# Optimization experiments

Measured on AMD Instinct MI355X. Metric: run time of the kernel, lower is better.

Reference implementation:

```python
import jax, jax.numpy as jnp
import numpy as np

K = 256      # embedding size k
STATE = 128  # latent state size
IN = 64      # external input size
OBS = 64     # observation size
L = 512      # sequence length (time-major)
B = 256      # batch size


def _glorot(key, shape):
    return jax.random.normal(key, shape, dtype=jnp.float32) / float(np.sqrt(shape[0]))


def setup_inputs():
    key = jax.random.key(0)
    ks = jax.random.split(key, 12)
    p = {}
    p["external_input_seq"] = jax.random.normal(ks[0], (L, B, IN), dtype=jnp.float32)
    p["observations_seq"] = jax.random.normal(ks[1], (L, B, OBS), dtype=jnp.float32)
    p["eps"] = jax.random.normal(ks[2], (L, B, STATE), dtype=jnp.float32)  # reparam noise
    # PreProcess: Linear + tanh
    p["Wu"] = _glorot(ks[3], (IN, K)); p["bu"] = jnp.zeros((K,), jnp.float32)
    p["Wx"] = _glorot(ks[4], (OBS, K)); p["bx"] = jnp.zeros((K,), jnp.float32)
    # input_rnn: vanilla tanh RNN, 1 layer, k -> k
    p["W_ih"] = _glorot(ks[5], (K, K)); p["b_ih"] = jnp.zeros((K,), jnp.float32)
    p["W_hh"] = _glorot(ks[6], (K, K)); p["b_hh"] = jnp.zeros((K,), jnp.float32)
    # posterior_a_layer: MLP(2k, k, k, 1) = Linear -> tanh -> Linear
    p["Wa1"] = _glorot(ks[7], (2 * K, K)); p["ba1"] = jnp.zeros((K,), jnp.float32)
    p["Wa2"] = _glorot(ks[8], (K, K)); p["ba2"] = jnp.zeros((K,), jnp.float32)

    def dblock_params(k1, in_dim, hid, out):
        kk = jax.random.split(k1, 4)
        return (_glorot(kk[0], (in_dim, hid)), jnp.zeros((hid,), jnp.float32),
                _glorot(kk[1], (in_dim, hid)), jnp.zeros((hid,), jnp.float32),
                _glorot(kk[2], (hid, out)), jnp.zeros((out,), jnp.float32),
                _glorot(kk[3], (hid, out)), jnp.zeros((out,), jnp.float32))

    names = ["f1_W", "f1_b", "f2_W", "f2_b", "mu_W", "mu_b", "ls_W", "ls_b"]
    for pref, kk in (("post_", ks[9]), ("prior_", ks[10])):
        vals = dblock_params(kk, STATE + K, 2 * K, STATE)
        for n, v in zip(names, vals):
            p[pref + n] = v
    return p


def _dblock(x, f1_W, f1_b, f2_W, f2_b, mu_W, mu_b, ls_W, ls_b):
    # TD-VAE DBlock: gated hidden, then mu / logsigma heads
    t = jnp.tanh(x @ f1_W + f1_b) * jax.nn.sigmoid(x @ f2_W + f2_b)
    return t @ mu_W + mu_b, t @ ls_W + ls_b


def reference(external_input_seq, observations_seq, eps, Wu, bu, Wx, bx,
              W_ih, b_ih, W_hh, b_hh, Wa1, ba1, Wa2, ba2,
              post_f1_W, post_f1_b, post_f2_W, post_f2_b, post_mu_W, post_mu_b, post_ls_W, post_ls_b,
              prior_f1_W, prior_f1_b, prior_f2_W, prior_f2_b, prior_mu_W, prior_mu_b, prior_ls_W, prior_ls_b):
    batch = external_input_seq.shape[1]
    u_emb = jnp.tanh(external_input_seq @ Wu + bu)   # [L,B,K]
    x_emb = jnp.tanh(observations_seq @ Wx + bx)     # [L,B,K]

    # input_rnn (tanh RNN) over time, d0 = 0 (memory_state=None)
    def rnn_step(d, x):
        d_new = jnp.tanh(x @ W_ih + b_ih + d @ W_hh + b_hh)
        return d_new, d_new
    d0 = jnp.zeros((batch, W_hh.shape[0]), dtype=u_emb.dtype)
    dn, d_seq = jax.lax.scan(rnn_step, d0, u_emb)    # dn [B,K], d_seq [L,B,K]

    # posterior_a_layer: pointwise MLP; flip(0) then flip(0) is a no-op for a pointwise map
    ad = jnp.concatenate([d_seq, x_emb], axis=-1)    # [L,B,2K]
    a_seq = jnp.tanh(ad @ Wa1 + ba1) @ Wa2 + ba2     # [L,B,K]

    state_size = post_mu_W.shape[1]
    z0 = jnp.zeros((batch, state_size), dtype=u_emb.dtype)

    def step(z_prev, inp):
        a_t, d_t, e_t = inp
        mean_res, logsigma = _dblock(jnp.concatenate([z_prev, a_t], axis=-1),
                                     post_f1_W, post_f1_b, post_f2_W, post_f2_b,
                                     post_mu_W, post_mu_b, post_ls_W, post_ls_b)
        prior_mean = _dblock(jnp.concatenate([z_prev, d_t], axis=-1),
                             prior_f1_W, prior_f1_b, prior_f2_W, prior_f2_b,
                             prior_mu_W, prior_mu_b, prior_ls_W, prior_ls_b)[0]
        mu = prior_mean + mean_res
        # cov = diag(exp(logsigma)) -> std = exp(0.5*logsigma); reparameterized sample
        z_new = mu + jnp.exp(0.5 * logsigma) * e_t
        return z_new, (mu, logsigma)

    zn, (state_mu, state_logsigma) = jax.lax.scan(step, z0, (a_seq, d_seq, eps))
    return state_mu, state_logsigma, dn, zn
```

## Files before the change

kernel.cpp:

```cpp
#include <hip/hip_runtime.h>

#define LSEQ 512
#define BATCH 256
#define KDIM 256
#define STATE 128

using f32x4  = __attribute__((ext_vector_type(4))) float;
using short8 = __attribute__((ext_vector_type(8))) short;
using u32x2  = __attribute__((ext_vector_type(2))) unsigned int;
using u32x4  = __attribute__((ext_vector_type(4))) unsigned int;

__device__ __forceinline__ float bf2f(unsigned short u){
  return __uint_as_float(((unsigned int)u) << 16);
}
__device__ __forceinline__ unsigned short f2bf(float f){
  unsigned int u = __float_as_uint(f);
  u += 0x7FFFu + ((u >> 16) & 1u);
  return (unsigned short)(u >> 16);
}
__device__ __forceinline__ float fast_tanh(float x){
  float ax = fabsf(x);
  float e  = __expf(2.0f * ax);
  float t  = 1.0f - 2.0f / (e + 1.0f);
  return copysignf(t, x);
}
__device__ __forceinline__ float fast_sig(float x){
  return 1.0f / (1.0f + __expf(-x));
}
__device__ __forceinline__ f32x4 mfma16(short8 a, short8 b, f32x4 c){
  return __builtin_amdgcn_mfma_f32_16x16x32_bf16(a, b, c, 0, 0, 0);
}

__device__ __forceinline__ int swz128 (int b){ return b ^ ((((b >> 7) & 7) << 4)); }
__device__ __forceinline__ int swz256 (int b){ return b ^ ((((b >> 8) & 7) << 4)); }
__device__ __forceinline__ int swz512 (int b){ return b ^ ((((b >> 9) & 7) << 4)); }

__device__ __forceinline__ void st_b128_ic(void* p, u32x4 v){
  asm volatile("global_store_dwordx4 %0, %1, off sc0 sc1" :: "v"(p), "v"(v) : "memory");
}
__device__ __forceinline__ void st_b64_ic(void* p, u32x2 v){
  asm volatile("global_store_dwordx2 %0, %1, off sc0 sc1" :: "v"(p), "v"(v) : "memory");
}
#define LD2_IC(dst, p) asm volatile("global_load_dwordx2 %0, %1, off sc0 sc1" : "=v"(dst) : "v"(p) : "memory")

__device__ __forceinline__ f32x4 cvt4(u32x2 q){
  f32x4 r;
  r[0] = __uint_as_float(q[0] << 16);
  r[1] = __uint_as_float(q[0] & 0xFFFF0000u);
  r[2] = __uint_as_float(q[1] << 16);
  r[3] = __uint_as_float(q[1] & 0xFFFF0000u);
  return r;
}

struct WDesc { const float* src; unsigned short* dst; int K, N, ld, rowoff, coloff; };
struct WDescs { WDesc d[24]; };

__global__ __launch_bounds__(256,4) void convert_weights(WDescs ds){
  WDesc w = ds.d[blockIdx.y];
  int total = w.K * w.N;
  int idx = blockIdx.x * 256 + threadIdx.x;
  if (idx < total){
    int n = idx / w.K;
    int k = idx - n * w.K;
    w.dst[idx] = f2bf(w.src[(size_t)(w.rowoff + k) * w.ld + w.coloff + n]);
  }
}

__global__ __launch_bounds__(256,1) void init_flags(int* flags){
  flags[blockIdx.x * 256 + threadIdx.x] = 0;
}

struct GArg {
  const void* A; const unsigned short* Bt; const float* bias; const float* bias2;
  unsigned short* C; int lda, ldc, coff, K, act, a_f32;
};
struct GArgs { GArg g[4]; };

__global__ __launch_bounds__(256,2) void gemm_multi(GArgs args){
  GArg ga = args.g[blockIdx.z];
  __shared__ __align__(16) unsigned short lsA[128*64];
  __shared__ __align__(16) unsigned short lsB[128*64];
  const int tid  = threadIdx.x;
  const int wave = tid >> 6, lane = tid & 63;
  const int col_l = lane & 15, rgrp = lane >> 4;
  const int m0 = blockIdx.x * 128, n0 = blockIdx.y * 128;
  const int wm = (wave >> 1) * 64, wn = (wave & 1) * 64;

  f32x4 acc[4][4];
  const f32x4 z4 = {0.f,0.f,0.f,0.f};
  #pragma unroll
  for (int i=0;i<4;i++){ acc[i][0]=z4; acc[i][1]=z4; acc[i][2]=z4; acc[i][3]=z4; }

  const int srow = tid >> 1;
  const int sbe  = (tid & 1) * 32;

  for (int k0 = 0; k0 < ga.K; k0 += 64){
    uint4 av[4], bv[4];
    if (ga.a_f32){
      const float* Ap = (const float*)ga.A + (size_t)(m0 + srow) * ga.lda + k0 + sbe;
      uint4 fv[8];
      #pragma unroll
      for (int i=0;i<8;i++) fv[i] = *(const uint4*)((const char*)Ap + i*16);
      #pragma unroll
      for (int i=0;i<4;i++){
        const float* f = (const float*)&fv[i*2];
        uint4 o;
        o.x = (unsigned)f2bf(f[0]) | ((unsigned)f2bf(f[1]) << 16);
        o.y = (unsigned)f2bf(f[2]) | ((unsigned)f2bf(f[3]) << 16);
        o.z = (unsigned)f2bf(f[4]) | ((unsigned)f2bf(f[5]) << 16);
        o.w = (unsigned)f2bf(f[6]) | ((unsigned)f2bf(f[7]) << 16);
        av[i] = o;
      }
    } else {
      const unsigned short* Ap = (const unsigned short*)ga.A + (size_t)(m0 + srow) * ga.lda + k0 + sbe;
      #pragma unroll
      for (int i=0;i<4;i++) av[i] = *(const uint4*)((const char*)Ap + i*16);
    }
    const unsigned short* Bp = ga.Bt + (size_t)(n0 + srow) * ga.K + k0 + sbe;
    #pragma unroll
    for (int i=0;i<4;i++) bv[i] = *(const uint4*)((const char*)Bp + i*16);

    __syncthreads();
    #pragma unroll
    for (int i=0;i<4;i++){
      *(uint4*)((char*)lsA + swz128(srow*128 + sbe*2 + i*16)) = av[i];
      *(uint4*)((char*)lsB + swz128(srow*128 + sbe*2 + i*16)) = bv[i];
    }
    __syncthreads();
    #pragma unroll
    for (int kk=0; kk<2; kk++){
      short8 af[4], bfr[4];
      #pragma unroll
      for (int mt=0; mt<4; mt++)
        af[mt] = *(const short8*)((const char*)lsA + swz128((wm + mt*16 + col_l)*128 + kk*64 + rgrp*16));
      #pragma unroll
      for (int nt=0; nt<4; nt++)
        bfr[nt] = *(const short8*)((const char*)lsB + swz128((wn + nt*16 + col_l)*128 + kk*64 + rgrp*16));
      #pragma unroll
      for (int mt=0; mt<4; mt++)
        #pragma unroll
        for (int nt=0; nt<4; nt++)
          acc[mt][nt] = mfma16(af[mt], bfr[nt], acc[mt][nt]);
    }
  }
  #pragma unroll
  for (int nt=0; nt<4; nt++){
    int col = n0 + wn + nt*16 + col_l;
    const float* bsrc = (col < 512) ? ga.bias : ga.bias2;
    float bb = bsrc ? bsrc[col & 511] : 0.0f;
    #pragma unroll
    for (int mt=0; mt<4; mt++){
      #pragma unroll
      for (int r=0; r<4; r++){
        int row = m0 + wm + mt*16 + rgrp*4 + r;
        float v = acc[mt][nt][r] + bb;
        if (ga.act == 1) v = fast_tanh(v);
        ga.C[(size_t)row * ga.ldc + ga.coff + col] = f2bf(v);
      }
    }
  }
}

__global__ __launch_bounds__(256,1) void rnn_chunk(
    const unsigned short* __restrict__ rnn_in,
    const unsigned short* __restrict__ Whh_t,
    const float* __restrict__ b_hh,
    unsigned short* __restrict__ cat_d,
    float* __restrict__ dn_out,
    unsigned short* __restrict__ d_state,
    int t0, int nsteps)
{
  __shared__ __align__(16) unsigned short dls[16*256];
  const int tid = threadIdx.x, wave = tid >> 6, lane = tid & 63;
  const int col_l = lane & 15, rgrp = lane >> 4;
  const int brow0 = blockIdx.x * 16;
  const int ncol = wave * 64;

  short8 bfr[4][8];
  #pragma unroll
  for (int nt=0; nt<4; nt++){
    const unsigned short* bp = Whh_t + (size_t)(ncol + nt*16 + col_l) * 256;
    #pragma unroll
    for (int kk=0; kk<8; kk++)
      bfr[nt][kk] = *(const short8*)(bp + kk*32 + rgrp*8);
  }
  float bias[4];
  #pragma unroll
  for (int nt=0; nt<4; nt++) bias[nt] = b_hh[ncol + nt*16 + col_l];

  if (t0 == 0){
    for (int i = tid; i < 16*256; i += 256){
      int row = i >> 8, col = i & 255;
      *(unsigned short*)((char*)dls + swz512(row*512 + col*2)) = 0;
    }
  } else {
    const unsigned short* ds = d_state + (size_t)brow0 * 256;
    for (int i = tid; i < 16*256; i += 256){
      int row = i >> 8, col = i & 255;
      *(unsigned short*)((char*)dls + swz512(row*512 + col*2)) = ds[row*256 + col];
    }
  }
  __syncthreads();

  for (int tl=0; tl<nsteps; tl++){
    unsigned short rv[4][4];
    const unsigned short* rp = rnn_in + (size_t)(tl*BATCH + brow0) * 256;
    #pragma unroll
    for (int nt=0; nt<4; nt++)
      #pragma unroll
      for (int r=0; r<4; r++)
        rv[nt][r] = rp[(size_t)(rgrp*4 + r)*256 + ncol + nt*16 + col_l];

    f32x4 acc[4];
    const f32x4 z4 = {0.f,0.f,0.f,0.f};
    acc[0]=z4; acc[1]=z4; acc[2]=z4; acc[3]=z4;
    #pragma unroll
    for (int kk=0; kk<8; kk++){
      short8 af = *(const short8*)((const char*)dls + swz512((lane & 15)*512 + kk*64 + rgrp*16));
      #pragma unroll
      for (int nt=0; nt<4; nt++)
        acc[nt] = mfma16(af, bfr[nt][kk], acc[nt]);
    }
    __syncthreads();
    #pragma unroll
    for (int nt=0; nt<4; nt++){
      #pragma unroll
      for (int r=0; r<4; r++){
        float h = acc[nt][r] + bf2f(rv[nt][r]) + bias[nt];
        float d = fast_tanh(h);
        int row = rgrp*4 + r, col = ncol + nt*16 + col_l;
        unsigned short db = f2bf(d);
        *(unsigned short*)((char*)dls + swz512(row*512 + col*2)) = db;
        cat_d[(size_t)(tl*BATCH + brow0 + row)*512 + col] = db;
        if (t0 + tl == LSEQ-1) dn_out[(size_t)(brow0 + row)*256 + col] = d;
      }
    }
    __syncthreads();
  }
  unsigned short* dso = d_state + (size_t)brow0 * 256;
  for (int i = tid; i < 16*256; i += 256){
    int row = i >> 8, col = i & 255;
    dso[row*256 + col] = *(const unsigned short*)((const char*)dls + swz512(row*512 + col*2));
  }
}

__global__ __launch_bounds__(512,1) void zrec_mb(
    const unsigned short* __restrict__ preP, const unsigned short* __restrict__ preQ,
    const unsigned short* __restrict__ Wzz,
    const unsigned short* __restrict__ W2,
    const float* __restrict__ pmub, const float* __restrict__ plsb, const float* __restrict__ qmub,
    const float* __restrict__ eps,
    float* __restrict__ out_mu, float* __restrict__ out_ls, float* __restrict__ out_zn,
    unsigned short* __restrict__ z_state,
    unsigned short* __restrict__ mb, int* __restrict__ flags,
    int t0, int nsteps, int fbase)
{
  __shared__ __align__(16) unsigned short zls[16*128];
  __shared__ __align__(16) unsigned short tls[16*256];
  const int tid = threadIdx.x, wave = tid >> 6, lane = tid & 63;
  const int col_l = lane & 15, rgrp = lane >> 4;
  const int bid = blockIdx.x;
  const int c   = (bid >> 3) & 3;
  const int g   = (bid & 7) + ((bid >> 5) << 3);
  const int brow0 = g * 16;
  const int NT2 = (c < 2) ? 2 : 1;

  const unsigned short* pre = (c < 2) ? preP : preQ;
  const int cb = (c & 1) * 256;

  short8 w1[2][2][4];
  {
    const unsigned short* wz = Wzz + (size_t)c * 65536;
    #pragma unroll
    for (int m=0; m<2; m++)
      #pragma unroll
      for (int nt=0; nt<2; nt++){
        int n = wave*32 + nt*16 + col_l;
        #pragma unroll
        for (int kk=0; kk<4; kk++)
          w1[m][nt][kk] = *(const short8*)(wz + (size_t)(m*256 + n)*128 + kk*32 + rgrp*8);
      }
  }
  short8 w2r[2][8];
  {
    const unsigned short* wp = W2 + (size_t)c * 65536;
    #pragma unroll
    for (int nt=0; nt<2; nt++){
      if (nt < NT2){
        int ccol = wave*(16*((c<2)?2:1)) + nt*16;
        int mat = (c < 2) ? (ccol >> 7) : 0;
        int n   = (ccol & 127) + col_l;
        #pragma unroll
        for (int kk=0; kk<8; kk++)
          w2r[nt][kk] = *(const short8*)(wp + (size_t)(mat*128 + n)*256 + kk*32 + rgrp*8);
      }
    }
  }
  int* const myflag = flags + (g*4 + c)*32;

  if (t0 == 0){
    for (int i = tid; i < 16*128; i += 512){
      int row = i >> 7, col = i & 127;
      *(unsigned short*)((char*)zls + swz256(row*256 + col*2)) = 0;
    }
  } else {
    const unsigned short* zs = z_state + (size_t)brow0 * 128;
    for (int i = tid; i < 16*128; i += 512){
      int row = i >> 7, col = i & 127;
      *(unsigned short*)((char*)zls + swz256(row*256 + col*2)) = zs[row*128 + col];
    }
  }
  __syncthreads();

  auto LD_PRE = [&](int tl, unsigned short (&pa_)[2][4], unsigned short (&pb_)[2][4]){
    const unsigned short* bA = pre + ((size_t)tl*BATCH + brow0)*1024 + cb;
    #pragma unroll
    for (int nt=0; nt<2; nt++)
      #pragma unroll
      for (int r=0; r<4; r++){
        int row = rgrp*4 + r, col = wave*32 + nt*16 + col_l;
        pa_[nt][r] = bA[(size_t)row*1024 + col];
        pb_[nt][r] = bA[(size_t)row*1024 + 512 + col];
      }
  };

  const int rrow = tid >> 5;
  const int rc0  = (tid & 31) * 4;
  const f32x4 bp4 = *(const f32x4*)(pmub + rc0);
  const f32x4 bl4 = *(const f32x4*)(plsb + rc0);
  const f32x4 bq4 = *(const f32x4*)(qmub + rc0);

  unsigned short pa0[2][4], pb0[2][4], pa1[2][4], pb1[2][4];
  LD_PRE(0, pa0, pb0);

  const f32x4 z4 = {0.f,0.f,0.f,0.f};
  for (int tl=0; tl<nsteps; ++tl){
    size_t growr = (size_t)(t0+tl)*BATCH + brow0 + rrow;
    f32x4 er = *(const f32x4*)(eps + growr*STATE + rc0);
    int nx = (tl+1 < nsteps) ? tl+1 : tl;
    LD_PRE(nx, pa1, pb1);

    short8 af1[4];
    #pragma unroll
    for (int kk=0; kk<4; kk++)
      af1[kk] = *(const short8*)((const char*)zls + swz256((lane & 15)*256 + kk*64 + rgrp*16));
    f32x4 a1[2][2];
    a1[0][0]=z4; a1[0][1]=z4; a1[1][0]=z4; a1[1][1]=z4;
    #pragma unroll
    for (int kk=0; kk<4; kk++)
      #pragma unroll
      for (int m=0; m<2; m++)
        #pragma unroll
        for (int nt=0; nt<2; nt++)
          a1[m][nt] = mfma16(af1[kk], w1[m][nt][kk], a1[m][nt]);

    #pragma unroll
    for (int nt=0; nt<2; nt++)
      #pragma unroll
      for (int r=0; r<4; r++){
        float h1 = a1[0][nt][r] + bf2f(pa0[nt][r]);
        float h2 = a1[1][nt][r] + bf2f(pb0[nt][r]);
        float tv = fast_tanh(h1) * fast_sig(h2);
        int row = rgrp*4 + r, tcol = wave*32 + nt*16 + col_l;
        *(unsigned short*)((char*)tls + swz512(row*512 + tcol*2)) = f2bf(tv);
      }
    __syncthreads();

    f32x4 a2[2];
    a2[0]=z4; a2[1]=z4;
    #pragma unroll
    for (int kk=0; kk<8; kk++){
      short8 af2 = *(const short8*)((const char*)tls + swz512((lane & 15)*512 + kk*64 + rgrp*16));
      #pragma unroll
      for (int nt=0; nt<2; nt++)
        if (nt < NT2) a2[nt] = mfma16(af2, w2r[nt][kk], a2[nt]);
    }
    __syncthreads();

    if (c < 2){
      #pragma unroll
      for (int nt=0; nt<2; nt++)
        #pragma unroll
        for (int r=0; r<4; r++)
          tls[(rgrp*4 + r)*256 + wave*32 + nt*16 + col_l] = f2bf(a2[nt][r]);
    } else {
      #pragma unroll
      for (int r=0; r<4; r++)
        tls[(rgrp*4 + r)*128 + wave*16 + col_l] = f2bf(a2[0][r]);
    }
    __syncthreads();

    unsigned short* slot = mb + (size_t)((g*2 + (tl & 1))*4 + c)*4096;
    if (c < 2){
      u32x4 v = *(const u32x4*)((const char*)tls + tid*16);
      st_b128_ic(slot + tid*8, v);
    } else {
      u32x2 v = *(const u32x2*)((const char*)tls + tid*8);
      st_b64_ic(slot + tid*4, v);
    }
    asm volatile("s_waitcnt vmcnt(0)" ::: "memory");
    __syncthreads();
    const int target = fbase + tl + 1;
    if (tid == 0)
      __hip_atomic_store(myflag, target, __ATOMIC_RELAXED, __HIP_MEMORY_SCOPE_AGENT);

    if (wave == 7 && lane < 3){
      const int* pf = flags + (g*4 + ((c + 1 + lane) & 3))*32;
      while (__hip_atomic_load(pf, __ATOMIC_RELAXED, __HIP_MEMORY_SCOPE_AGENT) < target)
        __builtin_amdgcn_s_sleep(1);
    }
    __syncthreads();

    const unsigned short* mbb = mb + (size_t)((g*2 + (tl & 1))*4)*4096;
    const unsigned short* s0 = mbb;
    const unsigned short* s1 = mbb + 4096;
    const unsigned short* s2 = mbb + 8192;
    const unsigned short* s3 = mbb + 12288;
    u32x2 q0,q1,q2,q3,q4,q5;
    LD2_IC(q0, s0 + rrow*256 + rc0);
    LD2_IC(q1, s1 + rrow*256 + rc0);
    LD2_IC(q2, s0 + rrow*256 + 128 + rc0);
    LD2_IC(q3, s1 + rrow*256 + 128 + rc0);
    LD2_IC(q4, s2 + rrow*128 + rc0);
    LD2_IC(q5, s3 + rrow*128 + rc0);
    asm volatile("s_waitcnt vmcnt(0)" ::: "memory");
    __builtin_amdgcn_sched_barrier(0);

    f32x4 mup = cvt4(q0) + cvt4(q1);
    f32x4 lsv = cvt4(q2) + cvt4(q3) + bl4;
    f32x4 muq = cvt4(q4) + cvt4(q5);
    f32x4 muv = (muq + bq4) + (mup + bp4);
    f32x4 zv;
    #pragma unroll
    for (int i=0; i<4; i++) zv[i] = muv[i] + __expf(0.5f * lsv[i]) * er[i];

    unsigned int lo = (unsigned)f2bf(zv[0]) | ((unsigned)f2bf(zv[1]) << 16);
    unsigned int hi = (unsigned)f2bf(zv[2]) | ((unsigned)f2bf(zv[3]) << 16);
    uint2 zp; zp.x = lo; zp.y = hi;
    *(uint2*)((char*)zls + swz256(rrow*256 + rc0*2)) = zp;
    if (c == 0){
      *(f32x4*)(out_mu + growr*STATE + rc0) = muv;
      *(f32x4*)(out_ls + growr*STATE + rc0) = lsv;
      if (t0 + tl == LSEQ-1)
        *(f32x4*)(out_zn + ((size_t)(brow0 + rrow))*STATE + rc0) = zv;
    }
    __syncthreads();

    #pragma unroll
    for (int nt=0; nt<2; nt++)
      #pragma unroll
      for (int r=0; r<4; r++){ pa0[nt][r] = pa1[nt][r]; pb0[nt][r] = pb1[nt][r]; }
  }

  if (c == 0){
    unsigned short* zso = z_state + (size_t)brow0 * 128;
    for (int i = tid; i < 16*128; i += 512){
      int row = i >> 7, col = i & 127;
      zso[row*128 + col] = *(const unsigned short*)((const char*)zls + swz256(row*256 + col*2));
    }
  }
}

extern "C" void kernel_launch(void* const* d_in, const int* in_sizes, int n_in,
                              void* d_out, int out_size, void* d_ws, size_t ws_size,
                              hipStream_t stream)
{
  const float* ext = (const float*)d_in[0];
  const float* obs = (const float*)d_in[1];
  const float* eps = (const float*)d_in[2];
  const float* Wu  = (const float*)d_in[3];
  const float* bu  = (const float*)d_in[4];
  const float* Wx  = (const float*)d_in[5];
  const float* bx  = (const float*)d_in[6];
  const float* W_ih= (const float*)d_in[7];
  const float* b_ih= (const float*)d_in[8];
  const float* W_hh= (const float*)d_in[9];
  const float* b_hh= (const float*)d_in[10];
  const float* Wa1 = (const float*)d_in[11];
  const float* ba1 = (const float*)d_in[12];
  const float* Wa2 = (const float*)d_in[13];
  const float* ba2 = (const float*)d_in[14];
  const float* pf1W= (const float*)d_in[15]; const float* pf1b = (const float*)d_in[16];
  const float* pf2W= (const float*)d_in[17]; const float* pf2b = (const float*)d_in[18];
  const float* pmuW= (const float*)d_in[19]; const float* pmub = (const float*)d_in[20];
  const float* plsW= (const float*)d_in[21]; const float* plsb = (const float*)d_in[22];
  const float* qf1W= (const float*)d_in[23]; const float* qf1b = (const float*)d_in[24];
  const float* qf2W= (const float*)d_in[25]; const float* qf2b = (const float*)d_in[26];
  const float* qmuW= (const float*)d_in[27]; const float* qmub = (const float*)d_in[28];

  int NC = 0;
  const int cands[7] = {1,2,4,8,16,32,64};
  size_t rows = 0;
  for (int ci=0; ci<7; ci++){
    size_t r = (size_t)(LSEQ/cands[ci])*BATCH;
    size_t elems = 2700000 + r*3072;
    if (elems * 2 <= ws_size){ NC = cands[ci]; rows = r; break; }
  }
  if (!NC) return;
  const int nsteps = LSEQ/NC;
  const int gx = (int)(rows/128);

  unsigned short* ws = (unsigned short*)d_ws;
  size_t off = 0;
  auto alloc = [&](size_t elems){
    unsigned short* p = ws + off;
    off += (elems + 127) & ~(size_t)127;
    return p;
  };

  unsigned short* Wu_t  = alloc(64*256);
  unsigned short* Wx_t  = alloc(64*256);
  unsigned short* Wih_t = alloc(256*256);
  unsigned short* Whh_t = alloc(256*256);
  unsigned short* Wa1_t = alloc(512*256);
  unsigned short* Wa2_t = alloc(256*256);
  unsigned short* fAp   = alloc(1024*256);
  unsigned short* fAq   = alloc(1024*256);
  unsigned short* Wzz   = alloc(4*2*256*128);
  unsigned short* W2z   = alloc(4*2*128*256);
  unsigned short* d_state = alloc(256*256);
  unsigned short* z_state = alloc(256*128);
  unsigned short* mbx  = alloc(16*2*4*4096);
  int*   flg  = (int*)alloc(4096);
  unsigned short* bufA  = alloc(rows*256);
  unsigned short* bufB  = alloc(rows*256);
  unsigned short* bufC  = alloc(rows*512);
  unsigned short* preP  = alloc(rows*1024);
  unsigned short* preQ  = alloc(rows*1024);
  if (off * sizeof(unsigned short) > ws_size) return;

  float* out_mu = (float*)d_out;
  float* out_ls = out_mu + (size_t)LSEQ*BATCH*STATE;
  float* out_dn = out_ls + (size_t)LSEQ*BATCH*STATE;
  float* out_zn = out_dn + (size_t)BATCH*KDIM;

  WDescs wd;
  int wi = 0;
  auto add = [&](const float* s, unsigned short* d, int Kk, int Nn, int ld, int ro, int co){
    wd.d[wi].src = s; wd.d[wi].dst = d; wd.d[wi].K = Kk; wd.d[wi].N = Nn;
    wd.d[wi].ld = ld; wd.d[wi].rowoff = ro; wd.d[wi].coloff = co; wi++;
  };
  add(Wu,   Wu_t,  64, 256, 256, 0, 0);
  add(Wx,   Wx_t,  64, 256, 256, 0, 0);
  add(W_ih, Wih_t, 256, 256, 256, 0, 0);
  add(W_hh, Whh_t, 256, 256, 256, 0, 0);
  add(Wa1,  Wa1_t, 512, 256, 256, 0, 0);
  add(Wa2,  Wa2_t, 256, 256, 256, 0, 0);
  add(pf1W, fAp,            256, 512, 512, 128, 0);
  add(pf2W, fAp + 512*256,  256, 512, 512, 128, 0);
  add(qf1W, fAq,            256, 512, 512, 128, 0);
  add(qf2W, fAq + 512*256,  256, 512, 512, 128, 0);
  for (int c=0; c<4; c++){
    const float* s1 = (c < 2) ? pf1W : qf1W;
    const float* s2 = (c < 2) ? pf2W : qf2W;
    add(s1, Wzz + (size_t)(c*2+0)*32768, 128, 256, 512, 0, (c&1)*256);
    add(s2, Wzz + (size_t)(c*2+1)*32768, 128, 256, 512, 0, (c&1)*256);
  }
  add(pmuW, W2z + (size_t)(0*2+0)*32768, 256, 128, 128, 0,   0);
  add(plsW, W2z + (size_t)(0*2+1)*32768, 256, 128, 128, 0,   0);
  add(pmuW, W2z + (size_t)(1*2+0)*32768, 256, 128, 128, 256, 0);
  add(plsW, W2z + (size_t)(1*2+1)*32768, 256, 128, 128, 256, 0);
  add(qmuW, W2z + (size_t)(2*2+0)*32768, 256, 128, 128, 0,   0);
  add(qmuW, W2z + (size_t)(3*2+0)*32768, 256, 128, 128, 256, 0);

  convert_weights<<<dim3(512,24), 256, 0, stream>>>(wd);
  init_flags<<<8, 256, 0, stream>>>(flg);

  for (int c=0; c<NC; ++c){
    const int t0 = c * nsteps;
    const size_t row0 = (size_t)t0 * BATCH;

    GArgs e{};
    e.g[0] = GArg{ext + row0*64, Wu_t, bu, bu, bufA, 64, 256, 0,   64, 1, 1};
    e.g[1] = GArg{obs + row0*64, Wx_t, bx, bx, bufC, 64, 512, 256, 64, 1, 1};
    gemm_multi<<<dim3(gx,2,2), 256, 0, stream>>>(e);

    GArgs rn{};
    rn.g[0] = GArg{bufA, Wih_t, b_ih, b_ih, bufB, 256, 256, 0, 256, 0, 0};
    gemm_multi<<<dim3(gx,2,1), 256, 0, stream>>>(rn);

    rnn_chunk<<<16, 256, 0, stream>>>(bufB, Whh_t, b_hh, bufC, out_dn, d_state, t0, nsteps);

    GArgs a1{};
    a1.g[0] = GArg{bufC, Wa1_t, ba1, ba1, bufA, 512, 256, 0, 512, 1, 0};
    gemm_multi<<<dim3(gx,2,1), 256, 0, stream>>>(a1);

    GArgs a2{};
    a2.g[0] = GArg{bufA, Wa2_t, ba2, ba2, bufB, 256, 256, 0, 256, 0, 0};
    gemm_multi<<<dim3(gx,2,1), 256, 0, stream>>>(a2);

    GArgs pr{};
    pr.g[0] = GArg{bufB, fAp, pf1b, pf2b, preP, 256, 1024, 0, 256, 0, 0};
    pr.g[1] = GArg{bufC, fAq, qf1b, qf2b, preQ, 512, 1024, 0, 256, 0, 0};
    gemm_multi<<<dim3(gx,8,2), 256, 0, stream>>>(pr);

    zrec_mb<<<64, 512, 0, stream>>>(preP, preQ, Wzz, W2z,
                                    pmub, plsb, qmub, eps, out_mu, out_ls, out_zn,
                                    z_state, mbx, flg, t0, nsteps, c*nsteps);
  }
}
```

Measured before the change: 3.902 ms.

## Replace flag-based cross-block sync with sequence-tagged mailbox payloads

Drops the separate per-block flag store, the vmcnt wait and the spin on flags. Each lane now writes its partial mu/logsigma data into the mailbox with the step number embedded in every 16-byte packet, and readers poll the packets until all tags match. The aim is to cut the latency of one publish-then-flag round trip per recurrent step and to remove a couple of block-wide barriers, using a separate LDS buffer. The cost is a larger mailbox, roughly twice the store traffic, and a correctness dependence on 16-byte stores being seen atomically.

```diff
diff --git a/kernel.cpp b/kernel.cpp
--- a/kernel.cpp
+++ b/kernel.cpp
@@ -7,7 +7,6 @@
 
 using f32x4  = __attribute__((ext_vector_type(4))) float;
 using short8 = __attribute__((ext_vector_type(8))) short;
-using u32x2  = __attribute__((ext_vector_type(2))) unsigned int;
 using u32x4  = __attribute__((ext_vector_type(4))) unsigned int;
 
 __device__ __forceinline__ float bf2f(unsigned short u){
@@ -18,6 +17,8 @@
   u += 0x7FFFu + ((u >> 16) & 1u);
   return (unsigned short)(u >> 16);
 }
+__device__ __forceinline__ float lo16f(unsigned u){ return __uint_as_float(u << 16); }
+__device__ __forceinline__ float hi16f(unsigned u){ return __uint_as_float(u & 0xFFFF0000u); }
 __device__ __forceinline__ float fast_tanh(float x){
   float ax = fabsf(x);
   float e  = __expf(2.0f * ax);
@@ -38,19 +39,7 @@
 __device__ __forceinline__ void st_b128_ic(void* p, u32x4 v){
   asm volatile("global_store_dwordx4 %0, %1, off sc0 sc1" :: "v"(p), "v"(v) : "memory");
 }
-__device__ __forceinline__ void st_b64_ic(void* p, u32x2 v){
-  asm volatile("global_store_dwordx2 %0, %1, off sc0 sc1" :: "v"(p), "v"(v) : "memory");
-}
-#define LD2_IC(dst, p) asm volatile("global_load_dwordx2 %0, %1, off sc0 sc1" : "=v"(dst) : "v"(p) : "memory")
-
-__device__ __forceinline__ f32x4 cvt4(u32x2 q){
-  f32x4 r;
-  r[0] = __uint_as_float(q[0] << 16);
-  r[1] = __uint_as_float(q[0] & 0xFFFF0000u);
-  r[2] = __uint_as_float(q[1] << 16);
-  r[3] = __uint_as_float(q[1] & 0xFFFF0000u);
-  return r;
-}
+#define LD4_IC(dst, p) asm volatile("global_load_dwordx4 %0, %1, off sc0 sc1" : "=v"(dst) : "v"(p) : "memory")
 
 struct WDesc { const float* src; unsigned short* dst; int K, N, ld, rowoff, coloff; };
 struct WDescs { WDesc d[24]; };
@@ -64,10 +53,6 @@
     int k = idx - n * w.K;
     w.dst[idx] = f2bf(w.src[(size_t)(w.rowoff + k) * w.ld + w.coloff + n]);
   }
-}
-
-__global__ __launch_bounds__(256,1) void init_flags(int* flags){
-  flags[blockIdx.x * 256 + threadIdx.x] = 0;
 }
 
 struct GArg {
@@ -252,11 +237,12 @@
     const float* __restrict__ eps,
     float* __restrict__ out_mu, float* __restrict__ out_ls, float* __restrict__ out_zn,
     unsigned short* __restrict__ z_state,
-    unsigned short* __restrict__ mb, int* __restrict__ flags,
+    unsigned short* __restrict__ mb,
     int t0, int nsteps, int fbase)
 {
   __shared__ __align__(16) unsigned short zls[16*128];
   __shared__ __align__(16) unsigned short tls[16*256];
+  __shared__ __align__(16) unsigned short bls[16*256];
   const int tid = threadIdx.x, wave = tid >> 6, lane = tid & 63;
   const int col_l = lane & 15, rgrp = lane >> 4;
   const int bid = blockIdx.x;
@@ -296,7 +282,6 @@
       }
     }
   }
-  int* const myflag = flags + (g*4 + c)*32;
 
   if (t0 == 0){
     for (int i = tid; i < 16*128; i += 512){
@@ -375,60 +360,83 @@
       for (int nt=0; nt<2; nt++)
         if (nt < NT2) a2[nt] = mfma16(af2, w2r[nt][kk], a2[nt]);
     }
-    __syncthreads();
-
     if (c < 2){
       #pragma unroll
       for (int nt=0; nt<2; nt++)
         #pragma unroll
         for (int r=0; r<4; r++)
-          tls[(rgrp*4 + r)*256 + wave*32 + nt*16 + col_l] = f2bf(a2[nt][r]);
+          bls[(rgrp*4 + r)*256 + wave*32 + nt*16 + col_l] = f2bf(a2[nt][r]);
     } else {
       #pragma unroll
       for (int r=0; r<4; r++)
-        tls[(rgrp*4 + r)*128 + wave*16 + col_l] = f2bf(a2[0][r]);
+        bls[(rgrp*4 + r)*128 + wave*16 + col_l] = f2bf(a2[0][r]);
     }
     __syncthreads();
 
-    unsigned short* slot = mb + (size_t)((g*2 + (tl & 1))*4 + c)*4096;
+    const int target = fbase + tl + 1;
+    unsigned short* slot = mb + (size_t)((g*2 + (tl & 1))*4 + c)*8192;
     if (c < 2){
-      u32x4 v = *(const u32x4*)((const char*)tls + tid*16);
-      st_b128_ic(slot + tid*8, v);
+      uint2 muw = *(const uint2*)&bls[rrow*256 + rc0];
+      unsigned lsw0 = *(const unsigned*)&bls[rrow*256 + 128 + rc0];
+      unsigned lsw1 = *(const unsigned*)&bls[rrow*256 + 128 + rc0 + 2];
+      u32x4 lA; lA[0]=muw.x; lA[1]=muw.y; lA[2]=lsw0; lA[3]=(unsigned)target;
+      u32x4 lB; lB[0]=lsw1; lB[1]=0; lB[2]=0; lB[3]=(unsigned)target;
+      st_b128_ic((char*)slot + tid*32,      lA);
+      st_b128_ic((char*)slot + tid*32 + 16, lB);
     } else {
-      u32x2 v = *(const u32x2*)((const char*)tls + tid*8);
-      st_b64_ic(slot + tid*4, v);
-    }
-    asm volatile("s_waitcnt vmcnt(0)" ::: "memory");
-    __syncthreads();
-    const int target = fbase + tl + 1;
-    if (tid == 0)
-      __hip_atomic_store(myflag, target, __ATOMIC_RELAXED, __HIP_MEMORY_SCOPE_AGENT);
-
-    if (wave == 7 && lane < 3){
-      const int* pf = flags + (g*4 + ((c + 1 + lane) & 3))*32;
-      while (__hip_atomic_load(pf, __ATOMIC_RELAXED, __HIP_MEMORY_SCOPE_AGENT) < target)
-        __builtin_amdgcn_s_sleep(1);
-    }
-    __syncthreads();
-
-    const unsigned short* mbb = mb + (size_t)((g*2 + (tl & 1))*4)*4096;
-    const unsigned short* s0 = mbb;
-    const unsigned short* s1 = mbb + 4096;
-    const unsigned short* s2 = mbb + 8192;
-    const unsigned short* s3 = mbb + 12288;
-    u32x2 q0,q1,q2,q3,q4,q5;
-    LD2_IC(q0, s0 + rrow*256 + rc0);
-    LD2_IC(q1, s1 + rrow*256 + rc0);
-    LD2_IC(q2, s0 + rrow*256 + 128 + rc0);
-    LD2_IC(q3, s1 + rrow*256 + 128 + rc0);
-    LD2_IC(q4, s2 + rrow*128 + rc0);
-    LD2_IC(q5, s3 + rrow*128 + rc0);
-    asm volatile("s_waitcnt vmcnt(0)" ::: "memory");
-    __builtin_amdgcn_sched_barrier(0);
-
-    f32x4 mup = cvt4(q0) + cvt4(q1);
-    f32x4 lsv = cvt4(q2) + cvt4(q3) + bl4;
-    f32x4 muq = cvt4(q4) + cvt4(q5);
+      uint2 qw = *(const uint2*)&bls[rrow*128 + rc0];
+      u32x4 lC; lC[0]=qw.x; lC[1]=qw.y; lC[2]=0; lC[3]=(unsigned)target;
+      st_b128_ic((char*)slot + tid*16, lC);
+    }
+
+    const unsigned short* mbB = mb + (size_t)((g*2 + (tl & 1))*4)*8192;
+    f32x4 p0mu, p0ls, p1mu, p1ls, q2v, q3v;
+    if (c < 2){
+      const char* pa = (const char*)(mbB + (size_t)(c^1)*8192) + tid*32;
+      const char* p2 = (const char*)(mbB + (size_t)2*8192) + tid*16;
+      const char* p3 = (const char*)(mbB + (size_t)3*8192) + tid*16;
+      u32x4 LA, LB, L2, L3;
+      for (;;){
+        LD4_IC(LA, pa); LD4_IC(LB, pa+16); LD4_IC(L2, p2); LD4_IC(L3, p3);
+        asm volatile("s_waitcnt vmcnt(0)" ::: "memory");
+        if ((int)LA[3]==target && (int)LB[3]==target && (int)L2[3]==target && (int)L3[3]==target) break;
+      }
+      f32x4 omu, ols, pmu_, pls_;
+      omu[0]=bf2f(bls[rrow*256+rc0+0]); omu[1]=bf2f(bls[rrow*256+rc0+1]);
+      omu[2]=bf2f(bls[rrow*256+rc0+2]); omu[3]=bf2f(bls[rrow*256+rc0+3]);
+      ols[0]=bf2f(bls[rrow*256+128+rc0+0]); ols[1]=bf2f(bls[rrow*256+128+rc0+1]);
+      ols[2]=bf2f(bls[rrow*256+128+rc0+2]); ols[3]=bf2f(bls[rrow*256+128+rc0+3]);
+      pmu_[0]=lo16f(LA[0]); pmu_[1]=hi16f(LA[0]); pmu_[2]=lo16f(LA[1]); pmu_[3]=hi16f(LA[1]);
+      pls_[0]=lo16f(LA[2]); pls_[1]=hi16f(LA[2]); pls_[2]=lo16f(LB[0]); pls_[3]=hi16f(LB[0]);
+      q2v[0]=lo16f(L2[0]); q2v[1]=hi16f(L2[0]); q2v[2]=lo16f(L2[1]); q2v[3]=hi16f(L2[1]);
+      q3v[0]=lo16f(L3[0]); q3v[1]=hi16f(L3[0]); q3v[2]=lo16f(L3[1]); q3v[3]=hi16f(L3[1]);
+      if (c == 0){ p0mu=omu; p0ls=ols; p1mu=pmu_; p1ls=pls_; }
+      else       { p1mu=omu; p1ls=ols; p0mu=pmu_; p0ls=pls_; }
+    } else {
+      const char* p0 = (const char*)(mbB) + tid*32;
+      const char* p1 = (const char*)(mbB + (size_t)8192) + tid*32;
+      const char* pq = (const char*)(mbB + (size_t)((c==2)?3:2)*8192) + tid*16;
+      u32x4 A0, A1, B0, B1, Q;
+      for (;;){
+        LD4_IC(A0, p0); LD4_IC(A1, p0+16); LD4_IC(B0, p1); LD4_IC(B1, p1+16); LD4_IC(Q, pq);
+        asm volatile("s_waitcnt vmcnt(0)" ::: "memory");
+        if ((int)A0[3]==target && (int)A1[3]==target && (int)B0[3]==target &&
+            (int)B1[3]==target && (int)Q[3]==target) break;
+      }
+      p0mu[0]=lo16f(A0[0]); p0mu[1]=hi16f(A0[0]); p0mu[2]=lo16f(A0[1]); p0mu[3]=hi16f(A0[1]);
+      p0ls[0]=lo16f(A0[2]); p0ls[1]=hi16f(A0[2]); p0ls[2]=lo16f(A1[0]); p0ls[3]=hi16f(A1[0]);
+      p1mu[0]=lo16f(B0[0]); p1mu[1]=hi16f(B0[0]); p1mu[2]=lo16f(B0[1]); p1mu[3]=hi16f(B0[1]);
+      p1ls[0]=lo16f(B0[2]); p1ls[1]=hi16f(B0[2]); p1ls[2]=lo16f(B1[0]); p1ls[3]=hi16f(B1[0]);
+      f32x4 oq, pq_;
+      oq[0]=bf2f(bls[rrow*128+rc0+0]); oq[1]=bf2f(bls[rrow*128+rc0+1]);
+      oq[2]=bf2f(bls[rrow*128+rc0+2]); oq[3]=bf2f(bls[rrow*128+rc0+3]);
+      pq_[0]=lo16f(Q[0]); pq_[1]=hi16f(Q[0]); pq_[2]=lo16f(Q[1]); pq_[3]=hi16f(Q[1]);
+      if (c == 2){ q2v=oq; q3v=pq_; } else { q3v=oq; q2v=pq_; }
+    }
+
+    f32x4 mup = p0mu + p1mu;
+    f32x4 lsv = p0ls + p1ls + bl4;
+    f32x4 muq = q2v + q3v;
     f32x4 muv = (muq + bq4) + (mup + bp4);
     f32x4 zv;
     #pragma unroll
@@ -493,7 +501,7 @@
   size_t rows = 0;
   for (int ci=0; ci<7; ci++){
     size_t r = (size_t)(LSEQ/cands[ci])*BATCH;
-    size_t elems = 2700000 + r*3072;
+    size_t elems = 3400000 + r*3072;
     if (elems * 2 <= ws_size){ NC = cands[ci]; rows = r; break; }
   }
   if (!NC) return;
@@ -520,8 +528,7 @@
   unsigned short* W2z   = alloc(4*2*128*256);
   unsigned short* d_state = alloc(256*256);
   unsigned short* z_state = alloc(256*128);
-  unsigned short* mbx  = alloc(16*2*4*4096);
-  int*   flg  = (int*)alloc(4096);
+  unsigned short* mbx  = alloc(16*2*4*8192);
   unsigned short* bufA  = alloc(rows*256);
   unsigned short* bufB  = alloc(rows*256);
   unsigned short* bufC  = alloc(rows*512);
@@ -564,7 +571,6 @@
   add(qmuW, W2z + (size_t)(3*2+0)*32768, 256, 128, 128, 256, 0);
 
   convert_weights<<<dim3(512,24), 256, 0, stream>>>(wd);
-  init_flags<<<8, 256, 0, stream>>>(flg);
 
   for (int c=0; c<NC; ++c){
     const int t0 = c * nsteps;
@@ -596,6 +602,6 @@
 
     zrec_mb<<<64, 512, 0, stream>>>(preP, preQ, Wzz, W2z,
                                     pmub, plsb, qmub, eps, out_mu, out_ls, out_zn,
-                                    z_state, mbx, flg, t0, nsteps, c*nsteps);
-  }
-}
+                                    z_state, mbx, t0, nsteps, c*nsteps);
+  }
+}
```

Measured after the change: 4.296 ms. 1.1x slower.

## Add double-buffered direct global-to-LDS GEMM for the bf16 projection GEMMs

Applied to the files above, without the earlier changes.

Adds a new GEMM kernel that stages A and B tiles straight into LDS with global_load_lds, double-buffered so the next K-slice loads while MFMAs run on the current one. The RNN input projection, posterior-a MLP and DBlock pre-activation GEMMs now use it instead of the register-staged gemm_multi. This targets exposed global-load latency and the VGPR round-trip in the tiled GEMMs, at the cost of 64KB of LDS per block and a larger workspace reservation, which may lower occupancy or force more chunks.

```diff
diff --git a/kernel.cpp b/kernel.cpp
--- a/kernel.cpp
+++ b/kernel.cpp
@@ -143,6 +143,95 @@
           acc[mt][nt] = mfma16(af[mt], bfr[nt], acc[mt][nt]);
     }
   }
+  #pragma unroll
+  for (int nt=0; nt<4; nt++){
+    int col = n0 + wn + nt*16 + col_l;
+    const float* bsrc = (col < 512) ? ga.bias : ga.bias2;
+    float bb = bsrc ? bsrc[col & 511] : 0.0f;
+    #pragma unroll
+    for (int mt=0; mt<4; mt++){
+      #pragma unroll
+      for (int r=0; r<4; r++){
+        int row = m0 + wm + mt*16 + rgrp*4 + r;
+        float v = acc[mt][nt][r] + bb;
+        if (ga.act == 1) v = fast_tanh(v);
+        ga.C[(size_t)row * ga.ldc + ga.coff + col] = f2bf(v);
+      }
+    }
+  }
+}
+
+struct GArg2 {
+  const unsigned short* A; const unsigned short* Bt; const float* bias; const float* bias2;
+  unsigned short* C; int lda, ldc, coff, K, act;
+};
+struct GArgs2 { GArg2 g[2]; };
+
+__global__ __launch_bounds__(256,2) void gemm_glds(GArgs2 args){
+  GArg2 ga = args.g[blockIdx.z];
+  __shared__ __align__(16) unsigned short ls[4][128*64];
+  const int tid  = threadIdx.x;
+  const int wave = tid >> 6, lane = tid & 63;
+  const int col_l = lane & 15, rgrp = lane >> 4;
+  const int m0 = blockIdx.x * 128, n0 = blockIdx.y * 128;
+  const int wm = (wave >> 1) * 64, wn = (wave & 1) * 64;
+
+  const int lrow = lane >> 3;
+  const int scol = (((lane & 7) ^ lrow) << 3);
+
+  auto STAGE = [&](int k0, int buf){
+    #pragma unroll
+    for (int c = 0; c < 4; c++){
+      int srow = wave*32 + c*8 + lrow;
+      const unsigned short* pa = ga.A  + (size_t)(m0 + srow) * ga.lda + k0 + scol;
+      const unsigned short* pb = ga.Bt + (size_t)(n0 + srow) * ga.K  + k0 + scol;
+      __builtin_amdgcn_global_load_lds(
+          (const __attribute__((address_space(1))) unsigned int*)pa,
+          (__attribute__((address_space(3))) unsigned int*)((char*)&ls[buf*2][0]   + wave*4096 + c*1024),
+          16, 0, 0);
+      __builtin_amdgcn_global_load_lds(
+          (const __attribute__((address_space(1))) unsigned int*)pb,
+          (__attribute__((address_space(3))) unsigned int*)((char*)&ls[buf*2+1][0] + wave*4096 + c*1024),
+          16, 0, 0);
+    }
+  };
+
+  f32x4 acc[4][4];
+  const f32x4 z4 = {0.f,0.f,0.f,0.f};
+  #pragma unroll
+  for (int i=0;i<4;i++){ acc[i][0]=z4; acc[i][1]=z4; acc[i][2]=z4; acc[i][3]=z4; }
+
+  const int niter = ga.K >> 6;
+  STAGE(0, 0);
+
+  for (int i = 0; i < niter; i++){
+    if (i + 1 < niter){
+      STAGE((i+1)*64, (i+1) & 1);
+      asm volatile("s_waitcnt vmcnt(8)" ::: "memory");
+    } else {
+      asm volatile("s_waitcnt vmcnt(0)" ::: "memory");
+    }
+    __syncthreads();
+    const char* la = (const char*)&ls[(i&1)*2][0];
+    const char* lb = (const char*)&ls[(i&1)*2+1][0];
+    #pragma unroll
+    for (int kk=0; kk<2; kk++){
+      short8 af[4], bfr[4];
+      #pragma unroll
+      for (int mt=0; mt<4; mt++)
+        af[mt] = *(const short8*)(la + swz128((wm + mt*16 + col_l)*128 + kk*64 + rgrp*16));
+      #pragma unroll
+      for (int nt=0; nt<4; nt++)
+        bfr[nt] = *(const short8*)(lb + swz128((wn + nt*16 + col_l)*128 + kk*64 + rgrp*16));
+      #pragma unroll
+      for (int mt=0; mt<4; mt++)
+        #pragma unroll
+        for (int nt=0; nt<4; nt++)
+          acc[mt][nt] = mfma16(af[mt], bfr[nt], acc[mt][nt]);
+    }
+    __syncthreads();
+  }
+
   #pragma unroll
   for (int nt=0; nt<4; nt++){
     int col = n0 + wn + nt*16 + col_l;
@@ -493,7 +582,7 @@
   size_t rows = 0;
   for (int ci=0; ci<7; ci++){
     size_t r = (size_t)(LSEQ/cands[ci])*BATCH;
-    size_t elems = 2700000 + r*3072;
+    size_t elems = 3400000 + r*3072;
     if (elems * 2 <= ws_size){ NC = cands[ci]; rows = r; break; }
   }
   if (!NC) return;
@@ -575,24 +664,24 @@
     e.g[1] = GArg{obs + row0*64, Wx_t, bx, bx, bufC, 64, 512, 256, 64, 1, 1};
     gemm_multi<<<dim3(gx,2,2), 256, 0, stream>>>(e);
 
-    GArgs rn{};
-    rn.g[0] = GArg{bufA, Wih_t, b_ih, b_ih, bufB, 256, 256, 0, 256, 0, 0};
-    gemm_multi<<<dim3(gx,2,1), 256, 0, stream>>>(rn);
+    GArgs2 rn{};
+    rn.g[0] = GArg2{bufA, Wih_t, b_ih, b_ih, bufB, 256, 256, 0, 256, 0};
+    gemm_glds<<<dim3(gx,2,1), 256, 0, stream>>>(rn);
 
     rnn_chunk<<<16, 256, 0, stream>>>(bufB, Whh_t, b_hh, bufC, out_dn, d_state, t0, nsteps);
 
-    GArgs a1{};
-    a1.g[0] = GArg{bufC, Wa1_t, ba1, ba1, bufA, 512, 256, 0, 512, 1, 0};
-    gemm_multi<<<dim3(gx,2,1), 256, 0, stream>>>(a1);
-
-    GArgs a2{};
-    a2.g[0] = GArg{bufA, Wa2_t, ba2, ba2, bufB, 256, 256, 0, 256, 0, 0};
-    gemm_multi<<<dim3(gx,2,1), 256, 0, stream>>>(a2);
-
-    GArgs pr{};
-    pr.g[0] = GArg{bufB, fAp, pf1b, pf2b, preP, 256, 1024, 0, 256, 0, 0};
-    pr.g[1] = GArg{bufC, fAq, qf1b, qf2b, preQ, 512, 1024, 0, 256, 0, 0};
-    gemm_multi<<<dim3(gx,8,2), 256, 0, stream>>>(pr);
+    GArgs2 a1{};
+    a1.g[0] = GArg2{bufC, Wa1_t, ba1, ba1, bufA, 512, 256, 0, 512, 1};
+    gemm_glds<<<dim3(gx,2,1), 256, 0, stream>>>(a1);
+
+    GArgs2 a2{};
+    a2.g[0] = GArg2{bufA, Wa2_t, ba2, ba2, bufB, 256, 256, 0, 256, 0};
+    gemm_glds<<<dim3(gx,2,1), 256, 0, stream>>>(a2);
+
+    GArgs2 pr{};
+    pr.g[0] = GArg2{bufB, fAp, pf1b, pf2b, preP, 256, 1024, 0, 256, 0};
+    pr.g[1] = GArg2{bufC, fAq, qf1b, qf2b, preQ, 512, 1024, 0, 256, 0};
+    gemm_glds<<<dim3(gx,8,2), 256, 0, stream>>>(pr);
 
     zrec_mb<<<64, 512, 0, stream>>>(preP, preQ, Wzz, W2z,
                                     pmub, plsb, qmub, eps, out_mu, out_ls, out_zn,
```

Result: faster. 3.622 ms (-7.2%).
